# Kernel optimization log

Hardware: AMD Instinct MI355X
Metric: run time of the kernel (lower is better)

## Reference

```python
import jax, jax.numpy as jnp
import numpy as np
from jax import lax

N_C = 2
T = 5
NE = 17   # equality constraints per (sample, t)
NV = 24   # variables per (sample, t): p(4), f(4), f_e(4), alpha1(2), alpha2(2), gamma(4), gamma_e(4)
ITERS = 400
B = 512

F_MASK = jnp.zeros((NV,), bool).at[4:8].set(True)     # L1-penalized coords (f)
NN_MASK = jnp.zeros((NV,), bool).at[12:24].set(True)  # nonneg coords (alpha1, alpha2, gamma, gamma_e)


def _conv(x, w, b):
    return lax.conv_general_dilated(x, w, (1, 1), 'VALID',
                                    dimension_numbers=('NCHW', 'OIHW', 'NCHW')) + b[None, :, None, None]


def _maxpool(x, k):
    return lax.reduce_window(x, -jnp.inf, lax.max, (1, 1, k, k), (1, 1, k, k), 'VALID')


def _encoder(img, cw1, cb1, cw2, cb2, w3, b3, w4, b4):
    h = jax.nn.relu(_maxpool(_conv(img, cw1, cb1), 2))   # (B,10,20,20)
    h = jax.nn.relu(_maxpool(_conv(h, cw2, cb2), 4))     # (B,20,4,4)
    h = h.reshape(h.shape[0], -1)                        # (B,320)
    h = jax.nn.relu(h @ w3.T + b3)                       # dropout is eval-mode identity
    return jax.nn.relu(h @ w4.T + b4)                    # (B,100)


def _mlp(h, w1, b1, w2, b2, w3, b3):
    h = jax.nn.relu(h @ w1.T + b1)  # dropout eval-mode identity
    h = jax.nn.relu(h @ w2.T + b2)
    return h @ w3.T + b3


def _build_Ab(r, ddr, fc, p_e, fc_e, v, p_r):
    # one (t)-slice: r(3), ddr(3), fc(8), p_e(4), fc_e(8), v(8), p_r(4) -> A(17,24), b(17)
    A = jnp.zeros((NE, NV))
    b = jnp.zeros((NE,))
    # force balance x: sum(f) + f_e0 + f_e1 = ddr0  (original f[:20] covers all 4 rows, f[20:] empty)
    A = A.at[0, 4:8].set(1.0).at[0, 8].set(1.0).at[0, 9].set(1.0)
    b = b.at[0].set(ddr[0])
    # force balance y: f_e2 + f_e3 = ddr1
    A = A.at[1, 10].set(1.0).at[1, 11].set(1.0)
    b = b.at[1].set(ddr[1])
    # torque balance
    A = A.at[2, 6].set(p_r[0] - r[0]).at[2, 4].set(-(p_r[2] - r[1]))
    A = A.at[2, 7].set(p_r[1] - r[0]).at[2, 5].set(-(p_r[3] - r[1]))
    A = A.at[2, 10].set(p_e[0] - r[0]).at[2, 8].set(-(p_e[2] - r[1]))
    A = A.at[2, 11].set(p_e[1] - r[0]).at[2, 9].set(-(p_e[3] - r[1]))
    b = b.at[2].set(ddr[2])
    for c in range(N_C):
        # p = alpha1*v_a + alpha2*v_b, alpha1+alpha2=1
        A = A.at[3 + 3 * c, c].set(1.0).at[3 + 3 * c, 12 + c].set(-v[2 * c]).at[3 + 3 * c, 14 + c].set(-v[2 * c + 2])
        A = A.at[4 + 3 * c, c + 2].set(1.0).at[4 + 3 * c, 12 + c].set(-v[2 * c + 1]).at[4 + 3 * c, 14 + c].set(-v[2 * c + 3])
        A = A.at[5 + 3 * c, 12 + c].set(1.0).at[5 + 3 * c, 14 + c].set(1.0)
        b = b.at[5 + 3 * c].set(1.0)
        # friction cone: f = gamma1*fc_a + gamma2*fc_b
        A = A.at[9 + 2 * c, 16 + c].set(fc[2 * c]).at[9 + 2 * c, 18 + c].set(fc[2 * c + 2]).at[9 + 2 * c, 4 + c].set(-1.0)
        A = A.at[10 + 2 * c, 16 + c].set(fc[2 * c + 1]).at[10 + 2 * c, 18 + c].set(fc[2 * c + 3]).at[10 + 2 * c, 6 + c].set(-1.0)
    # external force cones
    A = A.at[13, 20].set(fc_e[0]).at[13, 21].set(fc_e[2]).at[13, 8].set(-1.0)
    A = A.at[14, 20].set(fc_e[1]).at[14, 21].set(fc_e[3]).at[14, 10].set(-1.0)
    A = A.at[15, 22].set(fc_e[4]).at[15, 23].set(fc_e[6]).at[15, 9].set(-1.0)
    A = A.at[16, 22].set(fc_e[5]).at[16, 23].set(fc_e[7]).at[16, 11].set(-1.0)
    return A, b


def _specnorm(A):
    def body(i, u):
        u = A.T @ (A @ u)
        return u / (jnp.linalg.norm(u) + 1e-12)
    u = lax.fori_loop(0, 25, body, jnp.ones((A.shape[-1],), A.dtype))
    return jnp.linalg.norm(A @ u)


def _solve_lp(A, b):
    # batched: min ||f||_1  s.t.  A z = b,  z[nn] >= 0   via PDHG (Chambolle-Pock)
    P = A.shape[0]
    L = lax.stop_gradient(jax.vmap(_specnorm)(A))
    tau = (0.9 / (L + 1e-8))[:, None]
    sig = tau

    def step(carry, _):
        z, zb, y = carry
        y = y + sig * (jnp.einsum('pev,pv->pe', A, zb) - b)
        g = z - tau * jnp.einsum('pev,pe->pv', A, y)
        zn = jnp.where(F_MASK, jnp.sign(g) * jnp.maximum(jnp.abs(g) - tau, 0.0),
                       jnp.where(NN_MASK, jnp.maximum(g, 0.0), g))
        return (zn, 2.0 * zn - z, y), None

    z0 = jnp.zeros((P, NV))
    y0 = jnp.zeros((P, NE))
    (z, _, _), _ = lax.scan(step, (z0, z0, y0), None, length=ITERS)
    return z


def reference(xtraj, x, x_img, cw1, cb1, cw2, cb2, w3, b3, w4, b4,
              pw1, pb1, pw2, pb2, pw3, pb3, vw1, vb1, vw2, vb2, vw3, vb3):
    Bn = xtraj.shape[0]
    img = x_img.reshape(Bn, 1, 50, 50)
    e = _encoder(img, cw1, cb1, cw2, cb2, w3, b3, w4, b4)       # (B,100)
    h = jnp.concatenate([e, xtraj], axis=1)                     # (B,145)
    p_r = _mlp(h, pw1, pb1, pw2, pb2, pw3, pb3)                 # (B,20)
    v = _mlp(h, vw1, vb1, vw2, vb2, vw3, vb3)                   # (B,40)
    r = xtraj[:, :15].reshape(Bn, 3, T)
    ddr = xtraj[:, 30:45].reshape(Bn, 3, T)
    fc = x[:, 20:60].reshape(Bn, 8, T)
    p_e = x[:, 60:80].reshape(Bn, 4, T)
    fc_e = x[:, 80:120].reshape(Bn, 8, T)
    vM = v.reshape(Bn, 8, T)
    p_rM = p_r.reshape(Bn, 4, T)

    def flat(a):  # (B,d,T) -> (B*T, d)
        return jnp.swapaxes(a, 1, 2).reshape(Bn * T, a.shape[1])

    A, bvec = jax.vmap(_build_Ab)(flat(r), flat(ddr), flat(fc), flat(p_e), flat(fc_e), flat(vM), flat(p_rM))
    z = _solve_lp(A, bvec).reshape(Bn, T, NV)
    p = jnp.swapaxes(z[..., 0:4], 1, 2).reshape(Bn, 20)   # matches p.view(1,-1) C-order of (4,5)
    f = jnp.swapaxes(z[..., 4:8], 1, 2).reshape(Bn, 20)
    dp = p_r - x[:, 0:20]
    dv = v - x[:, 120:160]
    return 100.0 * jnp.concatenate([p, f, 10.0 * dp, 10.0 * dv], axis=1)  # (B,100)


def setup_inputs() -> dict:
    key = jax.random.key(0)
    ks = jax.random.split(key, 32)

    def rn(k, shape, s=0.05):
        return (s * jax.random.normal(k, shape)).astype(jnp.float32)

    return {
        'xtraj': rn(ks[0], (B, 45), 1.0),
        'x': rn(ks[1], (B, 160), 1.0),
        'x_img': rn(ks[2], (B, 2500), 1.0),
        'cw1': rn(ks[3], (10, 1, 11, 11)), 'cb1': rn(ks[4], (10,)),
        'cw2': rn(ks[5], (20, 10, 5, 5)), 'cb2': rn(ks[6], (20,)),
        'w3': rn(ks[7], (150, 320)), 'b3': rn(ks[8], (150,)),
        'w4': rn(ks[9], (100, 150)), 'b4': rn(ks[10], (100,)),
        'pw1': rn(ks[11], (100, 145)), 'pb1': rn(ks[12], (100,)),
        'pw2': rn(ks[13], (100, 100)), 'pb2': rn(ks[14], (100,)),
        'pw3': rn(ks[15], (20, 100)), 'pb3': rn(ks[16], (20,)),
        'vw1': rn(ks[17], (100, 145)), 'vb1': rn(ks[18], (100,)),
        'vw2': rn(ks[19], (100, 100)), 'vb2': rn(ks[20], (100,)),
        'vw3': rn(ks[21], (40, 100)), 'vb3': rn(ks[22], (40,)),
    }
```

## Files before the change

kernel.cpp:

```cpp
#include <hip/hip_runtime.h>

__global__ __launch_bounds__(128) void conv1_kernel(
    const float* __restrict__ x_img, const float* __restrict__ cw1,
    const float* __restrict__ cb1, float* __restrict__ h1)
{
    const int blk = blockIdx.x;
    const int b = blk >> 2;
    const int c = blk & 3;
    const int tid = threadIdx.x;

    __shared__ __align__(16) float s_img[1000];

    const float* img = x_img + (size_t)b * 2500 + (size_t)(10 * c) * 50;
    for (int i = tid; i < 1000; i += 128) s_img[i] = img[i];
    __syncthreads();

    if (tid < 100) {
        const int ly = tid / 20, px = tid % 20;
        const int py = 5 * c + ly;
        const int C = 2 * px;
        float acc0[10], acc1[10], acc2[10], acc3[10];
        #pragma unroll
        for (int oc = 0; oc < 10; ++oc) { acc0[oc] = 0.f; acc1[oc] = 0.f; acc2[oc] = 0.f; acc3[oc] = 0.f; }
        for (int r = 0; r < 12; ++r) {
            float v[12];
            #pragma unroll
            for (int j = 0; j < 6; ++j) {
                float2 t = *(const float2*)&s_img[(2 * ly + r) * 50 + C + 2 * j];
                v[2 * j] = t.x; v[2 * j + 1] = t.y;
            }
            if (r < 11) {
                #pragma unroll
                for (int oc = 0; oc < 10; ++oc) {
                    #pragma unroll
                    for (int kx = 0; kx < 11; ++kx) {
                        float w0 = cw1[oc * 121 + r * 11 + kx];
                        acc0[oc] = fmaf(v[kx], w0, acc0[oc]);
                        acc1[oc] = fmaf(v[kx + 1], w0, acc1[oc]);
                    }
                }
            }
            if (r >= 1) {
                #pragma unroll
                for (int oc = 0; oc < 10; ++oc) {
                    #pragma unroll
                    for (int kx = 0; kx < 11; ++kx) {
                        float w1 = cw1[oc * 121 + (r - 1) * 11 + kx];
                        acc2[oc] = fmaf(v[kx], w1, acc2[oc]);
                        acc3[oc] = fmaf(v[kx + 1], w1, acc3[oc]);
                    }
                }
            }
        }
        float* hb = h1 + (size_t)b * 4000 + py * 20 + px;
        #pragma unroll
        for (int oc = 0; oc < 10; ++oc) {
            float m = fmaxf(fmaxf(acc0[oc], acc1[oc]), fmaxf(acc2[oc], acc3[oc]));
            hb[oc * 400] = fmaxf(m + cb1[oc], 0.f);
        }
    }
}

__global__ __launch_bounds__(320) void head_kernel(
    const float* __restrict__ xtraj, const float* __restrict__ x,
    const float* __restrict__ h1g,
    const float* __restrict__ cw2, const float* __restrict__ cb2,
    const float* __restrict__ w3, const float* __restrict__ b3,
    const float* __restrict__ w4, const float* __restrict__ b4,
    const float* __restrict__ pw1, const float* __restrict__ pb1,
    const float* __restrict__ pw2, const float* __restrict__ pb2,
    const float* __restrict__ pw3, const float* __restrict__ pb3,
    const float* __restrict__ vw1, const float* __restrict__ vb1,
    const float* __restrict__ vw2, const float* __restrict__ vb2,
    const float* __restrict__ vw3, const float* __restrict__ vb3,
    float* __restrict__ out, float* __restrict__ ws_pr, float* __restrict__ ws_v)
{
    const int b = blockIdx.x;
    const int tid = threadIdx.x;

    __shared__ __align__(16) float s_h1[4000];
    __shared__ __align__(16) float s_w2[5000];
    __shared__ __align__(16) float s_h2[320];
    __shared__ float s_hc[145];
    __shared__ float s_t1[152];
    __shared__ float s_m1[256];
    __shared__ float s_m2[256];

    {
        const float4* src = (const float4*)(h1g + (size_t)b * 4000);
        float4* dst = (float4*)s_h1;
        for (int i = tid; i < 1000; i += 320) dst[i] = src[i];
        const float4* wsrc = (const float4*)cw2;
        float4* wdst = (float4*)s_w2;
        for (int i = tid; i < 1250; i += 320) wdst[i] = wsrc[i];
    }
    __syncthreads();

    {
        const int oc = tid >> 4, cell = tid & 15;
        const int R0 = (cell >> 2) * 4, C0 = (cell & 3) * 4;
        float acc[16];
        #pragma unroll
        for (int i = 0; i < 16; ++i) acc[i] = 0.f;
        for (int ic = 0; ic < 10; ++ic) {
            const float* hb = &s_h1[ic * 400];
            const float* wb = &s_w2[oc * 250 + ic * 25];
            float v[8][8];
            #pragma unroll
            for (int r = 0; r < 8; ++r) {
                float4 t0 = *(const float4*)&hb[(R0 + r) * 20 + C0];
                float4 t1 = *(const float4*)&hb[(R0 + r) * 20 + C0 + 4];
                v[r][0] = t0.x; v[r][1] = t0.y; v[r][2] = t0.z; v[r][3] = t0.w;
                v[r][4] = t1.x; v[r][5] = t1.y; v[r][6] = t1.z; v[r][7] = t1.w;
            }
            #pragma unroll
            for (int k = 0; k < 5; ++k) {
                #pragma unroll
                for (int kx = 0; kx < 5; ++kx) {
                    float wv = wb[k * 5 + kx];
                    #pragma unroll
                    for (int o = 0; o < 4; ++o) {
                        #pragma unroll
                        for (int cc = 0; cc < 4; ++cc)
                            acc[o * 4 + cc] = fmaf(v[o + k][cc + kx], wv, acc[o * 4 + cc]);
                    }
                }
            }
        }
        float m = acc[0];
        #pragma unroll
        for (int i = 1; i < 16; ++i) m = fmaxf(m, acc[i]);
        s_h2[tid] = fmaxf(m + cb2[oc], 0.f);
    }
    __syncthreads();

    if (tid < 150) {
        const float* w = w3 + tid * 320;
        float a0 = b3[tid], a1 = 0.f, a2 = 0.f, a3 = 0.f;
        for (int k = 0; k < 320; k += 4) {
            a0 = fmaf(s_h2[k],     w[k],     a0);
            a1 = fmaf(s_h2[k + 1], w[k + 1], a1);
            a2 = fmaf(s_h2[k + 2], w[k + 2], a2);
            a3 = fmaf(s_h2[k + 3], w[k + 3], a3);
        }
        s_t1[tid] = fmaxf((a0 + a1) + (a2 + a3), 0.f);
    }
    __syncthreads();

    if (tid < 100) {
        const float* w = w4 + tid * 150;
        float a0 = b4[tid], a1 = 0.f;
        for (int k = 0; k < 150; k += 2) {
            a0 = fmaf(s_t1[k],     w[k],     a0);
            a1 = fmaf(s_t1[k + 1], w[k + 1], a1);
        }
        s_hc[tid] = fmaxf(a0 + a1, 0.f);
    }
    if (tid >= 100 && tid < 145) s_hc[tid] = xtraj[b * 45 + (tid - 100)];
    __syncthreads();

    if (tid < 100) {
        const float* w = pw1 + tid * 145;
        float acc = pb1[tid];
        for (int k = 0; k < 145; ++k) acc = fmaf(s_hc[k], w[k], acc);
        s_m1[tid] = fmaxf(acc, 0.f);
    } else if (tid >= 128 && tid < 228) {
        int i = tid - 128;
        const float* w = vw1 + i * 145;
        float acc = vb1[i];
        for (int k = 0; k < 145; ++k) acc = fmaf(s_hc[k], w[k], acc);
        s_m1[tid] = fmaxf(acc, 0.f);
    }
    __syncthreads();

    if (tid < 100) {
        const float* w = pw2 + tid * 100;
        float acc = pb2[tid];
        for (int k = 0; k < 100; ++k) acc = fmaf(s_m1[k], w[k], acc);
        s_m2[tid] = fmaxf(acc, 0.f);
    } else if (tid >= 128 && tid < 228) {
        int i = tid - 128;
        const float* w = vw2 + i * 100;
        float acc = vb2[i];
        for (int k = 0; k < 100; ++k) acc = fmaf(s_m1[128 + k], w[k], acc);
        s_m2[tid] = fmaxf(acc, 0.f);
    }
    __syncthreads();

    if (tid < 20) {
        const float* w = pw3 + tid * 100;
        float acc = pb3[tid];
        for (int k = 0; k < 100; ++k) acc = fmaf(s_m2[k], w[k], acc);
        ws_pr[b * 20 + tid] = acc;
        out[b * 100 + 40 + tid] = 1000.f * (acc - x[b * 160 + tid]);
    } else if (tid >= 128 && tid < 168) {
        int i = tid - 128;
        const float* w = vw3 + i * 100;
        float acc = vb3[i];
        for (int k = 0; k < 100; ++k) acc = fmaf(s_m2[128 + k], w[k], acc);
        ws_v[b * 40 + i] = acc;
        out[b * 100 + 60 + i] = 1000.f * (acc - x[b * 160 + 120 + i]);
    }
}

__device__ const signed char AZ_IDX[32][8] = {
    {4,5,6,7,8,9,0,0},{10,11,0,0,0,0,0,0},{4,5,6,7,8,9,10,11},
    {0,12,14,0,0,0,0,0},{2,12,14,0,0,0,0,0},{12,14,0,0,0,0,0,0},
    {1,13,15,0,0,0,0,0},{3,13,15,0,0,0,0,0},{13,15,0,0,0,0,0,0},
    {16,18,4,0,0,0,0,0},{16,18,6,0,0,0,0,0},{17,19,5,0,0,0,0,0},
    {17,19,7,0,0,0,0,0},{20,21,8,0,0,0,0,0},{20,21,10,0,0,0,0,0},
    {22,23,9,0,0,0,0,0},{22,23,11,0,0,0,0,0},
    {0},{0},{0},{0},{0},{0},{0},{0},{0},{0},{0},{0},{0},{0},{0}
};
__device__ const signed char AZ_SEL[32][8] = {
    {1,1,1,1,1,1,0,0},{1,1,0,0,0,0,0,0},{3,4,5,6,7,8,9,10},
    {1,11,13,0,0,0,0,0},{1,12,14,0,0,0,0,0},{1,1,0,0,0,0,0,0},
    {1,13,15,0,0,0,0,0},{1,14,16,0,0,0,0,0},{1,1,0,0,0,0,0,0},
    {17,19,2,0,0,0,0,0},{18,20,2,0,0,0,0,0},{19,21,2,0,0,0,0,0},
    {20,22,2,0,0,0,0,0},{23,25,2,0,0,0,0,0},{24,26,2,0,0,0,0,0},
    {27,29,2,0,0,0,0,0},{28,30,2,0,0,0,0,0},
    {0},{0},{0},{0},{0},{0},{0},{0},{0},{0},{0},{0},{0},{0},{0}
};
__device__ const signed char AT_IDX[32][3] = {
    {3,0,0},{6,0,0},{4,0,0},{7,0,0},
    {0,2,9},{0,2,11},{0,2,10},{0,2,12},{0,2,13},{0,2,15},{1,2,14},{1,2,16},
    {3,4,5},{6,7,8},{3,4,5},{6,7,8},
    {9,10,0},{11,12,0},{9,10,0},{11,12,0},
    {13,14,0},{13,14,0},{15,16,0},{15,16,0},
    {0},{0},{0},{0},{0},{0},{0},{0}
};
__device__ const signed char M_IDX[32][10] = {
    {0,12,14,0,0,0,0,0,0,0},
    {1,13,15,0,0,0,0,0,0,0},
    {2,12,14,0,0,0,0,0,0,0},
    {3,13,15,0,0,0,0,0,0,0},
    {4,5,6,7,8,9,10,11,16,18},
    {4,5,6,7,8,9,10,11,17,19},
    {4,5,6,7,8,9,10,11,16,18},
    {4,5,6,7,8,9,10,11,17,19},
    {4,5,6,7,8,9,10,11,20,21},
    {4,5,6,7,8,9,10,11,22,23},
    {4,5,6,7,8,9,10,11,20,21},
    {4,5,6,7,8,9,10,11,22,23},
    {0,2,12,14,0,0,0,0,0,0},
    {1,3,13,15,0,0,0,0,0,0},
    {0,2,12,14,0,0,0,0,0,0},
    {1,3,13,15,0,0,0,0,0,0},
    {4,6,16,18,0,0,0,0,0,0},
    {5,7,17,19,0,0,0,0,0,0},
    {4,6,16,18,0,0,0,0,0,0},
    {5,7,17,19,0,0,0,0,0,0},
    {8,10,20,21,0,0,0,0,0,0},
    {8,10,20,21,0,0,0,0,0,0},
    {9,11,22,23,0,0,0,0,0,0},
    {9,11,22,23,0,0,0,0,0,0},
    {0},{0},{0},{0},{0},{0},{0},{0}
};
__device__ const signed char M_MSK[32][10] = {
    {1,1,1,0,0,0,0,0,0,0},
    {1,1,1,0,0,0,0,0,0,0},
    {1,1,1,0,0,0,0,0,0,0},
    {1,1,1,0,0,0,0,0,0,0},
    {1,1,1,1,1,1,1,1,1,1},
    {1,1,1,1,1,1,1,1,1,1},
    {1,1,1,1,1,1,1,1,1,1},
    {1,1,1,1,1,1,1,1,1,1},
    {1,1,1,1,1,1,1,1,1,1},
    {1,1,1,1,1,1,1,1,1,1},
    {1,1,1,1,1,1,1,1,1,1},
    {1,1,1,1,1,1,1,1,1,1},
    {1,1,1,1,0,0,0,0,0,0},
    {1,1,1,1,0,0,0,0,0,0},
    {1,1,1,1,0,0,0,0,0,0},
    {1,1,1,1,0,0,0,0,0,0},
    {1,1,1,1,0,0,0,0,0,0},
    {1,1,1,1,0,0,0,0,0,0},
    {1,1,1,1,0,0,0,0,0,0},
    {1,1,1,1,0,0,0,0,0,0},
    {1,1,1,1,0,0,0,0,0,0},
    {1,1,1,1,0,0,0,0,0,0},
    {1,1,1,1,0,0,0,0,0,0},
    {1,1,1,1,0,0,0,0,0,0},
    {0},{0},{0},{0},{0},{0},{0},{0}
};

__global__ __launch_bounds__(64) void lp_kernel(
    const float* __restrict__ xtraj, const float* __restrict__ x,
    const float* __restrict__ ws_pr, const float* __restrict__ ws_v,
    float* __restrict__ out, int nprob)
{
    const int g = threadIdx.x >> 5;
    const int l = threadIdx.x & 31;
    const int p = blockIdx.x * 2 + g;
    const int pc = p < nprob ? p : nprob - 1;
    const int b = pc / 5, t = pc % 5;
    const float* xt = xtraj + b * 45;
    const float* xb = x + b * 160;

    __shared__ float s_val[2][32];
    __shared__ float s_A[2][17][24];
    __shared__ float s_b[2][17];

    {
        float val = 0.f;
        if (l == 1) val = 1.f;
        else if (l == 2) val = -1.f;
        else if (l >= 3 && l <= 10) {
            float r0 = xt[t], r1 = xt[5 + t];
            switch (l) {
                case 3:  val = r1 - ws_pr[b * 20 + 10 + t]; break;
                case 4:  val = r1 - ws_pr[b * 20 + 15 + t]; break;
                case 5:  val = ws_pr[b * 20 + 0 + t] - r0;  break;
                case 6:  val = ws_pr[b * 20 + 5 + t] - r0;  break;
                case 7:  val = r1 - xb[60 + 10 + t]; break;
                case 8:  val = r1 - xb[60 + 15 + t]; break;
                case 9:  val = xb[60 + 0 + t] - r0;  break;
                default: val = xb[60 + 5 + t] - r0;  break;
            }
        }
        else if (l >= 11 && l <= 16) val = -ws_v[b * 40 + 5 * (l - 11) + t];
        else if (l >= 17 && l <= 22) val = xb[20 + 5 * (l - 17) + t];
        else if (l >= 23 && l <= 30) val = xb[80 + 5 * (l - 23) + t];
        s_val[g][l] = val;
    }
    for (int i = threadIdx.x; i < 2 * 17 * 24; i += 64) (&s_A[0][0][0])[i] = 0.f;
    __syncthreads();

    if (l < 17) {
        #pragma unroll
        for (int k = 0; k < 8; ++k) {
            int sel = AZ_SEL[l][k];
            if (sel != 0) s_A[g][l][(int)AZ_IDX[l][k]] = s_val[g][sel];
        }
        float bb = 0.f;
        if (l == 0) bb = xt[30 + t];
        else if (l == 1) bb = xt[35 + t];
        else if (l == 2) bb = xt[40 + t];
        else if (l == 5 || l == 8) bb = 1.f;
        s_b[g][l] = bb;
    }
    __syncthreads();

    float mcf[10];
    int midx[10];
    float cc = 0.f;
    #pragma unroll
    for (int k = 0; k < 10; ++k) { mcf[k] = 0.f; midx[k] = 0; }
    if (l < 24) {
        int e0 = AT_IDX[l][0], e1 = AT_IDX[l][1], e2 = AT_IDX[l][2];
        float a0 = s_A[g][e0][l], a1 = s_A[g][e1][l], a2 = s_A[g][e2][l];
        cc = a0 * s_b[g][e0] + a1 * s_b[g][e1] + a2 * s_b[g][e2];
        #pragma unroll
        for (int k = 0; k < 10; ++k) {
            int j = M_IDX[l][k];
            midx[k] = j;
            float m = a0 * s_A[g][e0][j] + a1 * s_A[g][e1][j] + a2 * s_A[g][e2][j];
            mcf[k] = (M_MSK[l][k] != 0) ? m : 0.f;
        }
    }

    const bool isF  = (l >= 4 && l < 8);
    const bool isNN = (l >= 12);

    float u = (l < 24) ? 1.f : 0.f;
    for (int it = 0; it < 25; ++it) {
        float w = 0.f;
        #pragma unroll
        for (int k = 0; k < 10; ++k) w = fmaf(mcf[k], __shfl(u, midx[k], 32), w);
        float s = w * w;
        s += __shfl_xor(s, 16, 32); s += __shfl_xor(s, 8, 32);
        s += __shfl_xor(s, 4, 32);  s += __shfl_xor(s, 2, 32);
        s += __shfl_xor(s, 1, 32);
        u = w / (sqrtf(s) + 1e-12f);
    }
    float tau;
    {
        float w = 0.f;
        #pragma unroll
        for (int k = 0; k < 10; ++k) w = fmaf(mcf[k], __shfl(u, midx[k], 32), w);
        float s2 = u * w;
        s2 += __shfl_xor(s2, 16, 32); s2 += __shfl_xor(s2, 8, 32);
        s2 += __shfl_xor(s2, 4, 32);  s2 += __shfl_xor(s2, 2, 32);
        s2 += __shfl_xor(s2, 1, 32);
        tau = 0.9f / (sqrtf(fmaxf(s2, 0.f)) + 1e-8f);
    }

    float zv = 0.f, zbv = 0.f, qv = 0.f;
    for (int it = 0; it < 400; ++it) {
        float s = 0.f;
        #pragma unroll
        for (int k = 0; k < 10; ++k) s = fmaf(mcf[k], __shfl(zbv, midx[k], 32), s);
        qv = fmaf(tau, s - cc, qv);

        float gg = fmaf(-tau, qv, zv);
        float st = copysignf(fmaxf(fabsf(gg) - tau, 0.f), gg);
        float nn = fmaxf(gg, 0.f);
        float zn = isF ? st : (isNN ? nn : gg);
        zbv = 2.f * zn - zv;
        zv = zn;
    }

    if (p < nprob) {
        float* ob = out + b * 100;
        if (l < 4)      ob[l * 5 + t]            = 100.f * zv;
        else if (l < 8) ob[20 + (l - 4) * 5 + t] = 100.f * zv;
    }
}

extern "C" void kernel_launch(void* const* d_in, const int* in_sizes, int n_in,
                              void* d_out, int out_size, void* d_ws, size_t ws_size,
                              hipStream_t stream) {
    const float* xtraj = (const float*)d_in[0];
    const float* x     = (const float*)d_in[1];
    const float* x_img = (const float*)d_in[2];
    const float* cw1 = (const float*)d_in[3];
    const float* cb1 = (const float*)d_in[4];
    const float* cw2 = (const float*)d_in[5];
    const float* cb2 = (const float*)d_in[6];
    const float* w3  = (const float*)d_in[7];
    const float* b3  = (const float*)d_in[8];
    const float* w4  = (const float*)d_in[9];
    const float* b4  = (const float*)d_in[10];
    const float* pw1 = (const float*)d_in[11];
    const float* pb1 = (const float*)d_in[12];
    const float* pw2 = (const float*)d_in[13];
    const float* pb2 = (const float*)d_in[14];
    const float* pw3 = (const float*)d_in[15];
    const float* pb3 = (const float*)d_in[16];
    const float* vw1 = (const float*)d_in[17];
    const float* vb1 = (const float*)d_in[18];
    const float* vw2 = (const float*)d_in[19];
    const float* vb2 = (const float*)d_in[20];
    const float* vw3 = (const float*)d_in[21];
    const float* vb3 = (const float*)d_in[22];

    float* out = (float*)d_out;
    const int Bn = in_sizes[0] / 45;

    float* ws_pr = (float*)d_ws;
    float* ws_v  = ws_pr + (size_t)Bn * 20;
    float* ws_h1 = ws_v + (size_t)Bn * 40;

    conv1_kernel<<<Bn * 4, 128, 0, stream>>>(x_img, cw1, cb1, ws_h1);

    head_kernel<<<Bn, 320, 0, stream>>>(
        xtraj, x, ws_h1, cw2, cb2, w3, b3, w4, b4,
        pw1, pb1, pw2, pb2, pw3, pb3, vw1, vb1, vw2, vb2, vw3, vb3,
        out, ws_pr, ws_v);

    const int nprob = Bn * 5;
    lp_kernel<<<(nprob + 1) / 2, 64, 0, stream>>>(xtraj, x, ws_pr, ws_v, out, nprob);
}
```

Measured before the change: 268.0 us.

## Fuse head MLP and LP solver into one kernel with tree-summed matvec

```diff
diff --git a/kernel.cpp b/kernel.cpp
--- a/kernel.cpp
+++ b/kernel.cpp
@@ -58,148 +58,6 @@
             float m = fmaxf(fmaxf(acc0[oc], acc1[oc]), fmaxf(acc2[oc], acc3[oc]));
             hb[oc * 400] = fmaxf(m + cb1[oc], 0.f);
         }
-    }
-}
-
-__global__ __launch_bounds__(320) void head_kernel(
-    const float* __restrict__ xtraj, const float* __restrict__ x,
-    const float* __restrict__ h1g,
-    const float* __restrict__ cw2, const float* __restrict__ cb2,
-    const float* __restrict__ w3, const float* __restrict__ b3,
-    const float* __restrict__ w4, const float* __restrict__ b4,
-    const float* __restrict__ pw1, const float* __restrict__ pb1,
-    const float* __restrict__ pw2, const float* __restrict__ pb2,
-    const float* __restrict__ pw3, const float* __restrict__ pb3,
-    const float* __restrict__ vw1, const float* __restrict__ vb1,
-    const float* __restrict__ vw2, const float* __restrict__ vb2,
-    const float* __restrict__ vw3, const float* __restrict__ vb3,
-    float* __restrict__ out, float* __restrict__ ws_pr, float* __restrict__ ws_v)
-{
-    const int b = blockIdx.x;
-    const int tid = threadIdx.x;
-
-    __shared__ __align__(16) float s_h1[4000];
-    __shared__ __align__(16) float s_w2[5000];
-    __shared__ __align__(16) float s_h2[320];
-    __shared__ float s_hc[145];
-    __shared__ float s_t1[152];
-    __shared__ float s_m1[256];
-    __shared__ float s_m2[256];
-
-    {
-        const float4* src = (const float4*)(h1g + (size_t)b * 4000);
-        float4* dst = (float4*)s_h1;
-        for (int i = tid; i < 1000; i += 320) dst[i] = src[i];
-        const float4* wsrc = (const float4*)cw2;
-        float4* wdst = (float4*)s_w2;
-        for (int i = tid; i < 1250; i += 320) wdst[i] = wsrc[i];
-    }
-    __syncthreads();
-
-    {
-        const int oc = tid >> 4, cell = tid & 15;
-        const int R0 = (cell >> 2) * 4, C0 = (cell & 3) * 4;
-        float acc[16];
-        #pragma unroll
-        for (int i = 0; i < 16; ++i) acc[i] = 0.f;
-        for (int ic = 0; ic < 10; ++ic) {
-            const float* hb = &s_h1[ic * 400];
-            const float* wb = &s_w2[oc * 250 + ic * 25];
-            float v[8][8];
-            #pragma unroll
-            for (int r = 0; r < 8; ++r) {
-                float4 t0 = *(const float4*)&hb[(R0 + r) * 20 + C0];
-                float4 t1 = *(const float4*)&hb[(R0 + r) * 20 + C0 + 4];
-                v[r][0] = t0.x; v[r][1] = t0.y; v[r][2] = t0.z; v[r][3] = t0.w;
-                v[r][4] = t1.x; v[r][5] = t1.y; v[r][6] = t1.z; v[r][7] = t1.w;
-            }
-            #pragma unroll
-            for (int k = 0; k < 5; ++k) {
-                #pragma unroll
-                for (int kx = 0; kx < 5; ++kx) {
-                    float wv = wb[k * 5 + kx];
-                    #pragma unroll
-                    for (int o = 0; o < 4; ++o) {
-                        #pragma unroll
-                        for (int cc = 0; cc < 4; ++cc)
-                            acc[o * 4 + cc] = fmaf(v[o + k][cc + kx], wv, acc[o * 4 + cc]);
-                    }
-                }
-            }
-        }
-        float m = acc[0];
-        #pragma unroll
-        for (int i = 1; i < 16; ++i) m = fmaxf(m, acc[i]);
-        s_h2[tid] = fmaxf(m + cb2[oc], 0.f);
-    }
-    __syncthreads();
-
-    if (tid < 150) {
-        const float* w = w3 + tid * 320;
-        float a0 = b3[tid], a1 = 0.f, a2 = 0.f, a3 = 0.f;
-        for (int k = 0; k < 320; k += 4) {
-            a0 = fmaf(s_h2[k],     w[k],     a0);
-            a1 = fmaf(s_h2[k + 1], w[k + 1], a1);
-            a2 = fmaf(s_h2[k + 2], w[k + 2], a2);
-            a3 = fmaf(s_h2[k + 3], w[k + 3], a3);
-        }
-        s_t1[tid] = fmaxf((a0 + a1) + (a2 + a3), 0.f);
-    }
-    __syncthreads();
-
-    if (tid < 100) {
-        const float* w = w4 + tid * 150;
-        float a0 = b4[tid], a1 = 0.f;
-        for (int k = 0; k < 150; k += 2) {
-            a0 = fmaf(s_t1[k],     w[k],     a0);
-            a1 = fmaf(s_t1[k + 1], w[k + 1], a1);
-        }
-        s_hc[tid] = fmaxf(a0 + a1, 0.f);
-    }
-    if (tid >= 100 && tid < 145) s_hc[tid] = xtraj[b * 45 + (tid - 100)];
-    __syncthreads();
-
-    if (tid < 100) {
-        const float* w = pw1 + tid * 145;
-        float acc = pb1[tid];
-        for (int k = 0; k < 145; ++k) acc = fmaf(s_hc[k], w[k], acc);
-        s_m1[tid] = fmaxf(acc, 0.f);
-    } else if (tid >= 128 && tid < 228) {
-        int i = tid - 128;
-        const float* w = vw1 + i * 145;
-        float acc = vb1[i];
-        for (int k = 0; k < 145; ++k) acc = fmaf(s_hc[k], w[k], acc);
-        s_m1[tid] = fmaxf(acc, 0.f);
-    }
-    __syncthreads();
-
-    if (tid < 100) {
-        const float* w = pw2 + tid * 100;
-        float acc = pb2[tid];
-        for (int k = 0; k < 100; ++k) acc = fmaf(s_m1[k], w[k], acc);
-        s_m2[tid] = fmaxf(acc, 0.f);
-    } else if (tid >= 128 && tid < 228) {
-        int i = tid - 128;
-        const float* w = vw2 + i * 100;
-        float acc = vb2[i];
-        for (int k = 0; k < 100; ++k) acc = fmaf(s_m1[128 + k], w[k], acc);
-        s_m2[tid] = fmaxf(acc, 0.f);
-    }
-    __syncthreads();
-
-    if (tid < 20) {
-        const float* w = pw3 + tid * 100;
-        float acc = pb3[tid];
-        for (int k = 0; k < 100; ++k) acc = fmaf(s_m2[k], w[k], acc);
-        ws_pr[b * 20 + tid] = acc;
-        out[b * 100 + 40 + tid] = 1000.f * (acc - x[b * 160 + tid]);
-    } else if (tid >= 128 && tid < 168) {
-        int i = tid - 128;
-        const float* w = vw3 + i * 100;
-        float acc = vb3[i];
-        for (int k = 0; k < 100; ++k) acc = fmaf(s_m2[128 + k], w[k], acc);
-        ws_v[b * 40 + i] = acc;
-        out[b * 100 + 60 + i] = 1000.f * (acc - x[b * 160 + 120 + i]);
     }
 }
 
@@ -284,62 +142,198 @@
     {0},{0},{0},{0},{0},{0},{0},{0}
 };
 
-__global__ __launch_bounds__(64) void lp_kernel(
+__global__ __launch_bounds__(320) void head_lp_kernel(
     const float* __restrict__ xtraj, const float* __restrict__ x,
-    const float* __restrict__ ws_pr, const float* __restrict__ ws_v,
-    float* __restrict__ out, int nprob)
+    const float* __restrict__ h1g,
+    const float* __restrict__ cw2, const float* __restrict__ cb2,
+    const float* __restrict__ w3, const float* __restrict__ b3,
+    const float* __restrict__ w4, const float* __restrict__ b4,
+    const float* __restrict__ pw1, const float* __restrict__ pb1,
+    const float* __restrict__ pw2, const float* __restrict__ pb2,
+    const float* __restrict__ pw3, const float* __restrict__ pb3,
+    const float* __restrict__ vw1, const float* __restrict__ vb1,
+    const float* __restrict__ vw2, const float* __restrict__ vb2,
+    const float* __restrict__ vw3, const float* __restrict__ vb3,
+    float* __restrict__ out)
 {
-    const int g = threadIdx.x >> 5;
-    const int l = threadIdx.x & 31;
-    const int p = blockIdx.x * 2 + g;
-    const int pc = p < nprob ? p : nprob - 1;
-    const int b = pc / 5, t = pc % 5;
+    const int b = blockIdx.x;
+    const int tid = threadIdx.x;
+
+    __shared__ __align__(16) float s_h1[4000];
+    __shared__ __align__(16) float s_w2[5000];
+    __shared__ __align__(16) float s_h2[320];
+    __shared__ float s_hc[145];
+    __shared__ float s_t1[152];
+    __shared__ float s_m1[256];
+    __shared__ float s_m2[256];
+
+    float* Lb = s_h1;
+    float* s_pr = Lb + 2285;
+    float* s_vv = Lb + 2305;
+
+    {
+        const float4* src = (const float4*)(h1g + (size_t)b * 4000);
+        float4* dst = (float4*)s_h1;
+        for (int i = tid; i < 1000; i += 320) dst[i] = src[i];
+        const float4* wsrc = (const float4*)cw2;
+        float4* wdst = (float4*)s_w2;
+        for (int i = tid; i < 1250; i += 320) wdst[i] = wsrc[i];
+    }
+    __syncthreads();
+
+    {
+        const int oc = tid >> 4, cell = tid & 15;
+        const int R0 = (cell >> 2) * 4, C0 = (cell & 3) * 4;
+        float acc[16];
+        #pragma unroll
+        for (int i = 0; i < 16; ++i) acc[i] = 0.f;
+        for (int ic = 0; ic < 10; ++ic) {
+            const float* hb = &s_h1[ic * 400];
+            const float* wb = &s_w2[oc * 250 + ic * 25];
+            float v[8][8];
+            #pragma unroll
+            for (int r = 0; r < 8; ++r) {
+                float4 t0 = *(const float4*)&hb[(R0 + r) * 20 + C0];
+                float4 t1 = *(const float4*)&hb[(R0 + r) * 20 + C0 + 4];
+                v[r][0] = t0.x; v[r][1] = t0.y; v[r][2] = t0.z; v[r][3] = t0.w;
+                v[r][4] = t1.x; v[r][5] = t1.y; v[r][6] = t1.z; v[r][7] = t1.w;
+            }
+            #pragma unroll
+            for (int k = 0; k < 5; ++k) {
+                #pragma unroll
+                for (int kx = 0; kx < 5; ++kx) {
+                    float wv = wb[k * 5 + kx];
+                    #pragma unroll
+                    for (int o = 0; o < 4; ++o) {
+                        #pragma unroll
+                        for (int cc = 0; cc < 4; ++cc)
+                            acc[o * 4 + cc] = fmaf(v[o + k][cc + kx], wv, acc[o * 4 + cc]);
+                    }
+                }
+            }
+        }
+        float m = acc[0];
+        #pragma unroll
+        for (int i = 1; i < 16; ++i) m = fmaxf(m, acc[i]);
+        s_h2[tid] = fmaxf(m + cb2[oc], 0.f);
+    }
+    __syncthreads();
+
+    if (tid < 150) {
+        const float* w = w3 + tid * 320;
+        float a0 = b3[tid], a1 = 0.f, a2 = 0.f, a3 = 0.f;
+        for (int k = 0; k < 320; k += 4) {
+            a0 = fmaf(s_h2[k],     w[k],     a0);
+            a1 = fmaf(s_h2[k + 1], w[k + 1], a1);
+            a2 = fmaf(s_h2[k + 2], w[k + 2], a2);
+            a3 = fmaf(s_h2[k + 3], w[k + 3], a3);
+        }
+        s_t1[tid] = fmaxf((a0 + a1) + (a2 + a3), 0.f);
+    }
+    __syncthreads();
+
+    if (tid < 100) {
+        const float* w = w4 + tid * 150;
+        float a0 = b4[tid], a1 = 0.f;
+        for (int k = 0; k < 150; k += 2) {
+            a0 = fmaf(s_t1[k],     w[k],     a0);
+            a1 = fmaf(s_t1[k + 1], w[k + 1], a1);
+        }
+        s_hc[tid] = fmaxf(a0 + a1, 0.f);
+    }
+    if (tid >= 100 && tid < 145) s_hc[tid] = xtraj[b * 45 + (tid - 100)];
+    __syncthreads();
+
+    if (tid < 100) {
+        const float* w = pw1 + tid * 145;
+        float acc = pb1[tid];
+        for (int k = 0; k < 145; ++k) acc = fmaf(s_hc[k], w[k], acc);
+        s_m1[tid] = fmaxf(acc, 0.f);
+    } else if (tid >= 128 && tid < 228) {
+        int i = tid - 128;
+        const float* w = vw1 + i * 145;
+        float acc = vb1[i];
+        for (int k = 0; k < 145; ++k) acc = fmaf(s_hc[k], w[k], acc);
+        s_m1[tid] = fmaxf(acc, 0.f);
+    }
+    __syncthreads();
+
+    if (tid < 100) {
+        const float* w = pw2 + tid * 100;
+        float acc = pb2[tid];
+        for (int k = 0; k < 100; ++k) acc = fmaf(s_m1[k], w[k], acc);
+        s_m2[tid] = fmaxf(acc, 0.f);
+    } else if (tid >= 128 && tid < 228) {
+        int i = tid - 128;
+        const float* w = vw2 + i * 100;
+        float acc = vb2[i];
+        for (int k = 0; k < 100; ++k) acc = fmaf(s_m1[128 + k], w[k], acc);
+        s_m2[tid] = fmaxf(acc, 0.f);
+    }
+    __syncthreads();
+
+    if (tid < 20) {
+        const float* w = pw3 + tid * 100;
+        float acc = pb3[tid];
+        for (int k = 0; k < 100; ++k) acc = fmaf(s_m2[k], w[k], acc);
+        s_pr[tid] = acc;
+        out[b * 100 + 40 + tid] = 1000.f * (acc - x[b * 160 + tid]);
+    } else if (tid >= 128 && tid < 168) {
+        int i = tid - 128;
+        const float* w = vw3 + i * 100;
+        float acc = vb3[i];
+        for (int k = 0; k < 100; ++k) acc = fmaf(s_m2[128 + k], w[k], acc);
+        s_vv[i] = acc;
+        out[b * 100 + 60 + i] = 1000.f * (acc - x[b * 160 + 120 + i]);
+    }
+    __syncthreads();
+
+    if (tid >= 160) return;
+    const int t = tid >> 5;
+    const int l = tid & 31;
     const float* xt = xtraj + b * 45;
     const float* xb = x + b * 160;
 
-    __shared__ float s_val[2][32];
-    __shared__ float s_A[2][17][24];
-    __shared__ float s_b[2][17];
+    float* val = Lb + t * 32;
+    float* Ag  = Lb + 160 + t * 408;
+    float* bg  = Lb + 2200 + t * 17;
 
     {
-        float val = 0.f;
-        if (l == 1) val = 1.f;
-        else if (l == 2) val = -1.f;
+        float v_ = 0.f;
+        if (l == 1) v_ = 1.f;
+        else if (l == 2) v_ = -1.f;
         else if (l >= 3 && l <= 10) {
             float r0 = xt[t], r1 = xt[5 + t];
             switch (l) {
-                case 3:  val = r1 - ws_pr[b * 20 + 10 + t]; break;
-                case 4:  val = r1 - ws_pr[b * 20 + 15 + t]; break;
-                case 5:  val = ws_pr[b * 20 + 0 + t] - r0;  break;
-                case 6:  val = ws_pr[b * 20 + 5 + t] - r0;  break;
-                case 7:  val = r1 - xb[60 + 10 + t]; break;
-                case 8:  val = r1 - xb[60 + 15 + t]; break;
-                case 9:  val = xb[60 + 0 + t] - r0;  break;
-                default: val = xb[60 + 5 + t] - r0;  break;
-            }
-        }
-        else if (l >= 11 && l <= 16) val = -ws_v[b * 40 + 5 * (l - 11) + t];
-        else if (l >= 17 && l <= 22) val = xb[20 + 5 * (l - 17) + t];
-        else if (l >= 23 && l <= 30) val = xb[80 + 5 * (l - 23) + t];
-        s_val[g][l] = val;
-    }
-    for (int i = threadIdx.x; i < 2 * 17 * 24; i += 64) (&s_A[0][0][0])[i] = 0.f;
-    __syncthreads();
-
+                case 3:  v_ = r1 - s_pr[10 + t]; break;
+                case 4:  v_ = r1 - s_pr[15 + t]; break;
+                case 5:  v_ = s_pr[0 + t] - r0;  break;
+                case 6:  v_ = s_pr[5 + t] - r0;  break;
+                case 7:  v_ = r1 - xb[60 + 10 + t]; break;
+                case 8:  v_ = r1 - xb[60 + 15 + t]; break;
+                case 9:  v_ = xb[60 + 0 + t] - r0;  break;
+                default: v_ = xb[60 + 5 + t] - r0;  break;
+            }
+        }
+        else if (l >= 11 && l <= 16) v_ = -s_vv[5 * (l - 11) + t];
+        else if (l >= 17 && l <= 22) v_ = xb[20 + 5 * (l - 17) + t];
+        else if (l >= 23 && l <= 30) v_ = xb[80 + 5 * (l - 23) + t];
+        val[l] = v_;
+    }
+    for (int i = l; i < 408; i += 32) Ag[i] = 0.f;
     if (l < 17) {
         #pragma unroll
         for (int k = 0; k < 8; ++k) {
             int sel = AZ_SEL[l][k];
-            if (sel != 0) s_A[g][l][(int)AZ_IDX[l][k]] = s_val[g][sel];
+            if (sel != 0) Ag[l * 24 + (int)AZ_IDX[l][k]] = val[sel];
         }
         float bb = 0.f;
         if (l == 0) bb = xt[30 + t];
         else if (l == 1) bb = xt[35 + t];
         else if (l == 2) bb = xt[40 + t];
         else if (l == 5 || l == 8) bb = 1.f;
-        s_b[g][l] = bb;
-    }
-    __syncthreads();
+        bg[l] = bb;
+    }
 
     float mcf[10];
     int midx[10];
@@ -348,13 +342,13 @@
     for (int k = 0; k < 10; ++k) { mcf[k] = 0.f; midx[k] = 0; }
     if (l < 24) {
         int e0 = AT_IDX[l][0], e1 = AT_IDX[l][1], e2 = AT_IDX[l][2];
-        float a0 = s_A[g][e0][l], a1 = s_A[g][e1][l], a2 = s_A[g][e2][l];
-        cc = a0 * s_b[g][e0] + a1 * s_b[g][e1] + a2 * s_b[g][e2];
+        float a0 = Ag[e0 * 24 + l], a1 = Ag[e1 * 24 + l], a2 = Ag[e2 * 24 + l];
+        cc = a0 * bg[e0] + a1 * bg[e1] + a2 * bg[e2];
         #pragma unroll
         for (int k = 0; k < 10; ++k) {
             int j = M_IDX[l][k];
             midx[k] = j;
-            float m = a0 * s_A[g][e0][j] + a1 * s_A[g][e1][j] + a2 * s_A[g][e2][j];
+            float m = a0 * Ag[e0 * 24 + j] + a1 * Ag[e1 * 24 + j] + a2 * Ag[e2 * 24 + j];
             mcf[k] = (M_MSK[l][k] != 0) ? m : 0.f;
         }
     }
@@ -364,9 +358,10 @@
 
     float u = (l < 24) ? 1.f : 0.f;
     for (int it = 0; it < 25; ++it) {
-        float w = 0.f;
-        #pragma unroll
-        for (int k = 0; k < 10; ++k) w = fmaf(mcf[k], __shfl(u, midx[k], 32), w);
+        float pd[10];
+        #pragma unroll
+        for (int k = 0; k < 10; ++k) pd[k] = mcf[k] * __shfl(u, midx[k], 32);
+        float w = (((pd[0] + pd[1]) + (pd[2] + pd[3])) + ((pd[4] + pd[5]) + (pd[6] + pd[7]))) + (pd[8] + pd[9]);
         float s = w * w;
         s += __shfl_xor(s, 16, 32); s += __shfl_xor(s, 8, 32);
         s += __shfl_xor(s, 4, 32);  s += __shfl_xor(s, 2, 32);
@@ -375,9 +370,10 @@
     }
     float tau;
     {
-        float w = 0.f;
-        #pragma unroll
-        for (int k = 0; k < 10; ++k) w = fmaf(mcf[k], __shfl(u, midx[k], 32), w);
+        float pd[10];
+        #pragma unroll
+        for (int k = 0; k < 10; ++k) pd[k] = mcf[k] * __shfl(u, midx[k], 32);
+        float w = (((pd[0] + pd[1]) + (pd[2] + pd[3])) + ((pd[4] + pd[5]) + (pd[6] + pd[7]))) + (pd[8] + pd[9]);
         float s2 = u * w;
         s2 += __shfl_xor(s2, 16, 32); s2 += __shfl_xor(s2, 8, 32);
         s2 += __shfl_xor(s2, 4, 32);  s2 += __shfl_xor(s2, 2, 32);
@@ -387,20 +383,22 @@
 
     float zv = 0.f, zbv = 0.f, qv = 0.f;
     for (int it = 0; it < 400; ++it) {
-        float s = 0.f;
-        #pragma unroll
-        for (int k = 0; k < 10; ++k) s = fmaf(mcf[k], __shfl(zbv, midx[k], 32), s);
+        float pd[10];
+        #pragma unroll
+        for (int k = 0; k < 10; ++k) pd[k] = mcf[k] * __shfl(zbv, midx[k], 32);
+        float s = (((pd[0] + pd[1]) + (pd[2] + pd[3])) + ((pd[4] + pd[5]) + (pd[6] + pd[7]))) + (pd[8] + pd[9]);
         qv = fmaf(tau, s - cc, qv);
 
         float gg = fmaf(-tau, qv, zv);
-        float st = copysignf(fmaxf(fabsf(gg) - tau, 0.f), gg);
+        float cl = fminf(fmaxf(gg, -tau), tau);
+        float st = gg - cl;
         float nn = fmaxf(gg, 0.f);
         float zn = isF ? st : (isNN ? nn : gg);
         zbv = 2.f * zn - zv;
         zv = zn;
     }
 
-    if (p < nprob) {
+    {
         float* ob = out + b * 100;
         if (l < 4)      ob[l * 5 + t]            = 100.f * zv;
         else if (l < 8) ob[20 + (l - 4) * 5 + t] = 100.f * zv;
@@ -437,17 +435,12 @@
     float* out = (float*)d_out;
     const int Bn = in_sizes[0] / 45;
 
-    float* ws_pr = (float*)d_ws;
-    float* ws_v  = ws_pr + (size_t)Bn * 20;
-    float* ws_h1 = ws_v + (size_t)Bn * 40;
+    float* ws_h1 = (float*)d_ws;
 
     conv1_kernel<<<Bn * 4, 128, 0, stream>>>(x_img, cw1, cb1, ws_h1);
 
-    head_kernel<<<Bn, 320, 0, stream>>>(
+    head_lp_kernel<<<Bn, 320, 0, stream>>>(
         xtraj, x, ws_h1, cw2, cb2, w3, b3, w4, b4,
         pw1, pb1, pw2, pb2, pw3, pb3, vw1, vb1, vw2, vb2, vw3, vb3,
-        out, ws_pr, ws_v);
-
-    const int nprob = Bn * 5;
-    lp_kernel<<<(nprob + 1) / 2, 64, 0, stream>>>(xtraj, x, ws_pr, ws_v, out, nprob);
+        out);
 }
```

New measurement: 272.2 us. No clear change (+1.6%).
